# Kernel optimization log

Measured on AMD Instinct MI355X. Metric: run time of the kernel, lower is better.

## Reference

```python
import jax, jax.numpy as jnp
import numpy as np

B = 8192
H = 1024            # hidden_size
A = 512             # alphabet_size
S = 2               # sequence_length
D_IN = A * S        # 1024, gate input dim
D1, D2 = H // 2, H // 3   # decoder dims: 512, 341
TEMP = 1.0


def _linear_params(key, out_d, in_d):
    kw, kb = jax.random.split(key)
    lim = 1.0 / np.sqrt(in_d)
    W = jax.random.uniform(kw, (out_d, in_d), minval=-lim, maxval=lim, dtype=jnp.float32)
    b = jax.random.uniform(kb, (out_d,), minval=-lim, maxval=lim, dtype=jnp.float32)
    return W, b


def setup_inputs() -> dict:
    key = jax.random.key(0)
    ks = jax.random.split(key, 16)
    inp = {
        'x': jax.random.normal(ks[0], (B, D_IN), dtype=jnp.float32),
        'h': jax.random.normal(ks[1], (B, H), dtype=jnp.float32),
        'c': jax.random.normal(ks[2], (B, H), dtype=jnp.float32),
    }
    names = [('W_fi', 'b_fi', H, D_IN), ('W_fh', 'b_fh', H, H),
             ('W_ii', 'b_ii', H, D_IN), ('W_ih', 'b_ih', H, H),
             ('W_si', 'b_si', H, D_IN), ('W_sh', 'b_sh', H, H),
             ('W_oi', 'b_oi', H, D_IN), ('W_oh', 'b_oh', H, H),
             ('W_d1', 'b_d1', D1, H), ('W_d2', 'b_d2', D2, D1),
             ('W_d3', 'b_d3', A, D2)]
    for k, (wn, bn, od, idm) in zip(ks[3:3 + len(names)], names):
        W, b = _linear_params(k, od, idm)
        inp[wn] = W
        inp[bn] = b
    return inp


def reference(x, h, c,
              W_fi, b_fi, W_fh, b_fh,
              W_ii, b_ii, W_ih, b_ih,
              W_si, b_si, W_sh, b_sh,
              W_oi, b_oi, W_oh, b_oh,
              W_d1, b_d1, W_d2, b_d2, W_d3, b_d3):
    def lin(v, W, b):
        return v @ W.T + b

    f = jax.nn.sigmoid(lin(x, W_fi, b_fi) + lin(h, W_fh, b_fh))
    i = jax.nn.sigmoid(lin(x, W_ii, b_ii) + lin(h, W_ih, b_ih))
    s = jnp.tanh(lin(x, W_si, b_si) + lin(h, W_sh, b_sh))
    o = jax.nn.sigmoid(lin(x, W_oi, b_oi) + lin(h, W_oh, b_oh))
    c_new = c * f + i * s
    h_new = o * jnp.tanh(c_new)
    d = jnp.tanh(lin(h_new, W_d1, b_d1))
    d = jnp.tanh(lin(d, W_d2, b_d2))
    d = jax.nn.softmax(lin(d, W_d3, b_d3) / TEMP, axis=-1)
    return h_new, d
```

## Files before the change

### kernel.cpp

```cpp
#include <hip/hip_runtime.h>
#include <cstdint>
#include <cstddef>


typedef _Float16 half_t;
typedef _Float16 half8 __attribute__((ext_vector_type(8)));
typedef _Float16 half4v __attribute__((ext_vector_type(4)));
typedef float float4v __attribute__((ext_vector_type(4)));

#define GLD_LDS16(gptr, lptr)                                                  \
  __builtin_amdgcn_global_load_lds(                                            \
      (const __attribute__((address_space(1))) void*)(gptr),                   \
      (__attribute__((address_space(3))) void*)(lptr), 16, 0, 0)

__device__ __forceinline__ float fsig(float x) {
  return 1.0f / (1.0f + __expf(-x));
}
__device__ __forceinline__ float ftanh_(float x) {
  const float e = __expf(2.0f * x);
  return 1.0f - 2.0f / (e + 1.0f);
}

__global__ __launch_bounds__(256) void gemm_gates(const half_t* __restrict__ A,
                                                  const half_t* __restrict__ Bw,
                                                  const float* __restrict__ bias,
                                                  const float* __restrict__ cin,
                                                  float* __restrict__ hout,
                                                  half_t* __restrict__ h2f) {
  constexpr int K = 2048;
  __shared__ alignas(16) half_t As[128 * 32];
  __shared__ alignas(16) half_t Bs[128 * 32];
  const int tid = threadIdx.x;
  const int lane = tid & 63;
  const int wave = tid >> 6;
  const int m = lane & 15;
  const int q = lane >> 4;
  const int sx = (m >> 1) & 3;

  const int bid = blockIdx.x;
  const int xcd = bid & 7;
  const int l = bid >> 3;
  const size_t tile_n = (size_t)((xcd << 2) | (l & 3)) * 128;
  const size_t tile_m = (size_t)(l >> 2) * 128;
  const int wm = (wave >> 1) * 64;
  const int wn = (wave & 1) * 64;

  const int cA0 = tid, rA0 = cA0 >> 2, kA0 = ((cA0 & 3) ^ ((rA0 >> 1) & 3));
  const int cA1 = 256 + tid, rA1 = cA1 >> 2, kA1 = ((cA1 & 3) ^ ((rA1 >> 1) & 3));
  const half_t* Ag0 = A + (tile_m + rA0) * (size_t)K + kA0 * 8;
  const half_t* Ag1 = A + (tile_m + rA1) * (size_t)K + kA1 * 8;
  const half_t* Bg0 = Bw + (tile_n + rA0) * (size_t)K + kA0 * 8;
  const half_t* Bg1 = Bw + (tile_n + rA1) * (size_t)K + kA1 * 8;
  const int p0 = cA0 * 16, p1 = cA1 * 16;

  float4v acc[4][4] = {};
  for (int k0 = 0; k0 < K; k0 += 32) {
    __syncthreads();
    GLD_LDS16(Ag0 + k0, (char*)As + p0);
    GLD_LDS16(Ag1 + k0, (char*)As + p1);
    GLD_LDS16(Bg0 + k0, (char*)Bs + p0);
    GLD_LDS16(Bg1 + k0, (char*)Bs + p1);
    __syncthreads();
    const int ks = (q ^ sx) * 8;
    half8 af[4], bf[4];
#pragma unroll
    for (int i = 0; i < 4; ++i)
      af[i] = *(const half8*)(As + (wm + i * 16 + m) * 32 + ks);
#pragma unroll
    for (int j = 0; j < 4; ++j)
      bf[j] = *(const half8*)(Bs + (wn + j * 16 + m) * 32 + ks);
#pragma unroll
    for (int i = 0; i < 4; ++i)
#pragma unroll
      for (int j = 0; j < 4; ++j)
        acc[i][j] =
            __builtin_amdgcn_mfma_f32_16x16x32_f16(af[i], bf[j], acc[i][j], 0, 0, 0);
  }

  const int nwave = (int)tile_n + wn;
  const int u = ((nwave >> 6) << 4) + m;
  const int rtb = (int)((tile_m + wm) >> 4);
  const int ubase = (u >> 5) * 512 + ((u >> 3) & 3) * 128 + (u & 7);
  float bg[4];
#pragma unroll
  for (int g = 0; g < 4; ++g) bg[g] = bias[nwave + g * 16 + m];
#pragma unroll
  for (int i = 0; i < 4; ++i) {
#pragma unroll
    for (int r = 0; r < 4; ++r) {
      const size_t row = tile_m + wm + q * 4 + i * 16 + r;
      const size_t off = row * 1024 + u;
      const float F = fsig(acc[i][0][r] + bg[0]);
      const float I = fsig(acc[i][1][r] + bg[1]);
      const float S = ftanh_(acc[i][2][r] + bg[2]);
      const float O = fsig(acc[i][3][r] + bg[3]);
      const float cn = cin[off] * F + I * S;
      const float hn = O * ftanh_(cn);
      hout[off] = hn;
      h2f[(size_t)(rtb + i) * 16384 + ubase + (q * 4 + r) * 8] = (half_t)hn;
    }
  }
}

template <int K, int OUTK, int MODE>
__global__ __launch_bounds__(256) void dec_layer(const half_t* __restrict__ Af,
                                                 const half_t* __restrict__ W,
                                                 const float* __restrict__ bias,
                                                 void* __restrict__ outp) {
  constexpr int KP = K + 8;
  constexpr int CH = K / 8;
  constexpr int ITER = 32 * CH / 256;
  __shared__ alignas(16) half_t Wl[32 * KP];
  const int tid = threadIdx.x;
  const int lane = tid & 63;
  const int w = tid >> 6;
  const int m = lane & 15;
  const int q = lane >> 4;
  const int g = blockIdx.x;

#pragma unroll
  for (int it = 0; it < ITER; ++it) {
    const int ci = it * 256 + tid;
    const int c = ci / CH;
    const int kq = ci - c * CH;
    const half8 v = *(const half8*)(W + ((size_t)(g * 32 + c)) * K + kq * 8);
    *(half8*)(Wl + c * KP + kq * 8) = v;
  }
  __syncthreads();

  const int rt0 = blockIdx.y * 8 + w * 2;
  const half_t* a0 = Af + (size_t)rt0 * (16 * K) + lane * 8;
  const half_t* a1 = a0 + 16 * K;
  float4v acc[2][2] = {};
#pragma unroll 2
  for (int kk = 0; kk < K; kk += 32) {
    const half8 af0 = *(const half8*)(a0 + kk * 16);
    const half8 af1 = *(const half8*)(a1 + kk * 16);
    half8 bf[2];
#pragma unroll
    for (int j = 0; j < 2; ++j)
      bf[j] = *(const half8*)(Wl + (j * 16 + m) * KP + kk + q * 8);
    acc[0][0] = __builtin_amdgcn_mfma_f32_16x16x32_f16(af0, bf[0], acc[0][0], 0, 0, 0);
    acc[0][1] = __builtin_amdgcn_mfma_f32_16x16x32_f16(af0, bf[1], acc[0][1], 0, 0, 0);
    acc[1][0] = __builtin_amdgcn_mfma_f32_16x16x32_f16(af1, bf[0], acc[1][0], 0, 0, 0);
    acc[1][1] = __builtin_amdgcn_mfma_f32_16x16x32_f16(af1, bf[1], acc[1][1], 0, 0, 0);
  }

#pragma unroll
  for (int t = 0; t < 2; ++t) {
    const int rt = rt0 + t;
#pragma unroll
    for (int j = 0; j < 2; ++j) {
      const int col = g * 32 + j * 16 + m;
      const float bv = bias[col];
      if (MODE == 0) {
        half_t* of = (half_t*)outp;
        const size_t base = (size_t)rt * (16 * OUTK) + g * 512 +
                            (j * 2 + (m >> 3)) * 128 + (m & 7);
#pragma unroll
        for (int r = 0; r < 4; ++r)
          of[base + (q * 4 + r) * 8] = (half_t)ftanh_(acc[t][j][r] + bv);
      } else {
        float* ol = (float*)outp;
#pragma unroll
        for (int r = 0; r < 4; ++r)
          ol[((size_t)rt * 16 + q * 4 + r) * 512 + col] = acc[t][j][r] + bv;
      }
    }
  }
}

__global__ __launch_bounds__(256) void softmax512(const float* __restrict__ logits,
                                                  float* __restrict__ out) {
  const int row = blockIdx.x * 4 + (threadIdx.x >> 6);
  const int lane = threadIdx.x & 63;
  const float4v* src = (const float4v*)(logits + (size_t)row * 512);
  const float4v v0 = src[lane * 2];
  const float4v v1 = src[lane * 2 + 1];
  float mx = fmaxf(fmaxf(fmaxf(v0.x, v0.y), fmaxf(v0.z, v0.w)),
                   fmaxf(fmaxf(v1.x, v1.y), fmaxf(v1.z, v1.w)));
#pragma unroll
  for (int off = 32; off > 0; off >>= 1) mx = fmaxf(mx, __shfl_xor(mx, off, 64));
  const float e0 = __expf(v0.x - mx), e1 = __expf(v0.y - mx);
  const float e2 = __expf(v0.z - mx), e3 = __expf(v0.w - mx);
  const float e4 = __expf(v1.x - mx), e5 = __expf(v1.y - mx);
  const float e6 = __expf(v1.z - mx), e7 = __expf(v1.w - mx);
  float sum = ((e0 + e1) + (e2 + e3)) + ((e4 + e5) + (e6 + e7));
#pragma unroll
  for (int off = 32; off > 0; off >>= 1) sum += __shfl_xor(sum, off, 64);
  const float inv = 1.0f / sum;
  float4v o0, o1;
  o0.x = e0 * inv; o0.y = e1 * inv; o0.z = e2 * inv; o0.w = e3 * inv;
  o1.x = e4 * inv; o1.y = e5 * inv; o1.z = e6 * inv; o1.w = e7 * inv;
  float4v* dst = (float4v*)(out + (size_t)row * 512);
  dst[lane * 2] = o0;
  dst[lane * 2 + 1] = o1;
}

__global__ void prep_pack(const float* __restrict__ x, const float* __restrict__ h,
                          const float* __restrict__ Wfi, const float* __restrict__ Wfh,
                          const float* __restrict__ Wii, const float* __restrict__ Wih,
                          const float* __restrict__ Wsi, const float* __restrict__ Wsh,
                          const float* __restrict__ Woi, const float* __restrict__ Woh,
                          half_t* __restrict__ xh, half_t* __restrict__ wall) {
  const int bid = blockIdx.x;
  const float* src;
  half_t* dst;
  size_t idx;
  if (bid < 16384) {
    idx = ((size_t)bid * 256 + threadIdx.x) * 4;
    const size_t b = idx >> 11;
    const int col = (int)(idx & 2047);
    src = (col < 1024) ? (x + b * 1024 + col) : (h + b * 1024 + (col - 1024));
    dst = xh + idx;
  } else {
    idx = ((size_t)(bid - 16384) * 256 + threadIdx.x) * 4;
    const int n = (int)(idx >> 11);
    const int col = (int)(idx & 2047);
    const int g = (n >> 4) & 3;
    const size_t u = (size_t)(((n >> 6) << 4) | (n & 15));
    const float* Wi = (g == 0) ? Wfi : (g == 1) ? Wii : (g == 2) ? Wsi : Woi;
    const float* Wh = (g == 0) ? Wfh : (g == 1) ? Wih : (g == 2) ? Wsh : Woh;
    src = (col < 1024) ? (Wi + u * 1024 + col) : (Wh + u * 1024 + (col - 1024));
    dst = wall + idx;
  }
  const float4v v = *(const float4v*)src;
  half4v o;
  o.x = (half_t)v.x; o.y = (half_t)v.y; o.z = (half_t)v.z; o.w = (half_t)v.w;
  *(half4v*)dst = o;
}

__global__ void prep_small(const float* __restrict__ Wd1, const float* __restrict__ Wd2,
                           const float* __restrict__ Wd3, const float* __restrict__ bd2,
                           const float* __restrict__ bfi, const float* __restrict__ bfh,
                           const float* __restrict__ bii, const float* __restrict__ bih,
                           const float* __restrict__ bsi, const float* __restrict__ bsh,
                           const float* __restrict__ boi, const float* __restrict__ boh,
                           half_t* __restrict__ WD1, half_t* __restrict__ WD2h,
                           half_t* __restrict__ WD3h, float* __restrict__ BALL,
                           float* __restrict__ BD2) {
  const int bid = blockIdx.x;
  const int tid = threadIdx.x;
  if (bid < 512) {
    const size_t i4 = ((size_t)bid * 256 + tid) * 4;
    const float4v v = *(const float4v*)(Wd1 + i4);
    half4v o;
    o.x = (half_t)v.x; o.y = (half_t)v.y; o.z = (half_t)v.z; o.w = (half_t)v.w;
    *(half4v*)(WD1 + i4) = o;
  } else if (bid < 704) {
    const size_t i4 = ((size_t)(bid - 512) * 256 + tid) * 4;
    const int r = (int)(i4 >> 9);
    const int cc = (int)(i4 & 511);
    half4v o;
    if (r < 341) {
      const float4v v = *(const float4v*)(Wd2 + (size_t)r * 512 + cc);
      o.x = (half_t)v.x; o.y = (half_t)v.y; o.z = (half_t)v.z; o.w = (half_t)v.w;
    } else {
      o.x = (half_t)0.f; o.y = (half_t)0.f; o.z = (half_t)0.f; o.w = (half_t)0.f;
    }
    *(half4v*)(WD2h + i4) = o;
  } else if (bid < 896) {
    const size_t i4 = ((size_t)(bid - 704) * 256 + tid) * 4;
    const int r = (int)(i4 / 384);
    const int cc = (int)(i4 - (size_t)r * 384);
    half4v o;
    o.x = (cc + 0 < 341) ? (half_t)Wd3[(size_t)r * 341 + cc + 0] : (half_t)0.f;
    o.y = (cc + 1 < 341) ? (half_t)Wd3[(size_t)r * 341 + cc + 1] : (half_t)0.f;
    o.z = (cc + 2 < 341) ? (half_t)Wd3[(size_t)r * 341 + cc + 2] : (half_t)0.f;
    o.w = (cc + 3 < 341) ? (half_t)Wd3[(size_t)r * 341 + cc + 3] : (half_t)0.f;
    *(half4v*)(WD3h + i4) = o;
  } else if (bid < 912) {
    const int n = (bid - 896) * 256 + tid;
    const int g = (n >> 4) & 3;
    const int u = ((n >> 6) << 4) | (n & 15);
    const float* bi = (g == 0) ? bfi : (g == 1) ? bii : (g == 2) ? bsi : boi;
    const float* bh = (g == 0) ? bfh : (g == 1) ? bih : (g == 2) ? bsh : boh;
    BALL[n] = bi[u] + bh[u];
  } else {
    const int i = (bid - 912) * 256 + tid;
    if (i < 384) BD2[i] = (i < 341) ? bd2[i] : 0.0f;
  }
}

extern "C" void kernel_launch(void* const* d_in, const int* in_sizes, int n_in,
                              void* d_out, int out_size, void* d_ws, size_t ws_size,
                              hipStream_t stream) {
  const float* x = (const float*)d_in[0];
  const float* h = (const float*)d_in[1];
  const float* c = (const float*)d_in[2];
  const float* Wfi = (const float*)d_in[3];  const float* bfi = (const float*)d_in[4];
  const float* Wfh = (const float*)d_in[5];  const float* bfh = (const float*)d_in[6];
  const float* Wii = (const float*)d_in[7];  const float* bii = (const float*)d_in[8];
  const float* Wih = (const float*)d_in[9];  const float* bih = (const float*)d_in[10];
  const float* Wsi = (const float*)d_in[11]; const float* bsi = (const float*)d_in[12];
  const float* Wsh = (const float*)d_in[13]; const float* bsh = (const float*)d_in[14];
  const float* Woi = (const float*)d_in[15]; const float* boi = (const float*)d_in[16];
  const float* Woh = (const float*)d_in[17]; const float* boh = (const float*)d_in[18];
  const float* Wd1 = (const float*)d_in[19]; const float* bd1 = (const float*)d_in[20];
  const float* Wd2 = (const float*)d_in[21]; const float* bd2 = (const float*)d_in[22];
  const float* Wd3 = (const float*)d_in[23]; const float* bd3 = (const float*)d_in[24];

  char* ws = (char*)d_ws;
  size_t o = 0;
  auto alloc = [&](size_t bytes) {
    size_t cur = o;
    o += (bytes + 255) & ~(size_t)255;
    return cur;
  };
  half_t* XH   = (half_t*)(ws + alloc((size_t)8192 * 2048 * 2));
  half_t* WALL = (half_t*)(ws + alloc((size_t)4096 * 2048 * 2));
  float*  BALL = (float*)(ws + alloc(4096 * 4));
  half_t* WD1  = (half_t*)(ws + alloc((size_t)512 * 1024 * 2));
  half_t* WD2  = (half_t*)(ws + alloc((size_t)384 * 512 * 2));
  float*  BD2  = (float*)(ws + alloc(384 * 4));
  half_t* WD3  = (half_t*)(ws + alloc((size_t)512 * 384 * 2));
  half_t* H2F  = (half_t*)(ws + alloc((size_t)8192 * 1024 * 2));
  half_t* D1F  = (half_t*)(ws + alloc((size_t)8192 * 512 * 2));
  half_t* D2F  = (half_t*)(ws + alloc((size_t)8192 * 384 * 2));
  float*  LOG  = (float*)XH;

  float* h_out = (float*)d_out;
  float* d_outp = (float*)d_out + (size_t)8192 * 1024;

  prep_pack<<<24576, 256, 0, stream>>>(x, h, Wfi, Wfh, Wii, Wih, Wsi, Wsh, Woi, Woh,
                                       XH, WALL);
  prep_small<<<914, 256, 0, stream>>>(Wd1, Wd2, Wd3, bd2, bfi, bfh, bii, bih, bsi, bsh,
                                      boi, boh, WD1, WD2, WD3, BALL, BD2);

  gemm_gates<<<2048, 256, 0, stream>>>(XH, WALL, BALL, c, h_out, H2F);

  dec_layer<1024, 512, 0><<<dim3(16, 64), 256, 0, stream>>>(H2F, WD1, bd1, D1F);
  dec_layer<512, 384, 0><<<dim3(12, 64), 256, 0, stream>>>(D1F, WD2, BD2, D2F);
  dec_layer<384, 512, 1><<<dim3(16, 64), 256, 0, stream>>>(D2F, WD3, bd3, LOG);
  softmax512<<<2048, 256, 0, stream>>>(LOG, d_outp);
}
```

Baseline: 440.0 us.

## Enlarge gate GEMM tiles to 256x256 with triple-buffered async LDS pipeline

The fused gate GEMM moves from 128x128 tiles with 256 threads to 256x256 tiles with 512 threads, and each wave now computes a 128x64 sub-tile. Global-to-LDS loads become triple-buffered, prefetching two k-steps ahead and interleaving them with MFMA phases using explicit waitcnt, barriers and setprio. This targets the single-buffered load/compute serialization and the low reuse of the smaller tile. In exchange it uses much more LDS and more accumulator registers per thread, which can lower occupancy.

```diff
diff --git a/kernel.cpp b/kernel.cpp
--- a/kernel.cpp
+++ b/kernel.cpp
@@ -21,60 +21,110 @@
   return 1.0f - 2.0f / (e + 1.0f);
 }
 
-__global__ __launch_bounds__(256) void gemm_gates(const half_t* __restrict__ A,
-                                                  const half_t* __restrict__ Bw,
-                                                  const float* __restrict__ bias,
-                                                  const float* __restrict__ cin,
-                                                  float* __restrict__ hout,
-                                                  half_t* __restrict__ h2f) {
+__global__ __launch_bounds__(512, 2) void gemm_gates(const half_t* __restrict__ A,
+                                                     const half_t* __restrict__ Bw,
+                                                     const float* __restrict__ bias,
+                                                     const float* __restrict__ cin,
+                                                     float* __restrict__ hout,
+                                                     half_t* __restrict__ h2f) {
   constexpr int K = 2048;
-  __shared__ alignas(16) half_t As[128 * 32];
-  __shared__ alignas(16) half_t Bs[128 * 32];
+  constexpr int NT = 64;
+  __shared__ alignas(16) half_t As[3][256 * 32];
+  __shared__ alignas(16) half_t Bs[3][256 * 32];
   const int tid = threadIdx.x;
   const int lane = tid & 63;
   const int wave = tid >> 6;
   const int m = lane & 15;
   const int q = lane >> 4;
-  const int sx = (m >> 1) & 3;
+  const int ks = (q ^ ((m >> 1) & 3)) << 3;
+  const int wm = (wave >> 2) << 7;
+  const int wn = (wave & 3) << 6;
 
   const int bid = blockIdx.x;
   const int xcd = bid & 7;
   const int l = bid >> 3;
-  const size_t tile_n = (size_t)((xcd << 2) | (l & 3)) * 128;
-  const size_t tile_m = (size_t)(l >> 2) * 128;
-  const int wm = (wave >> 1) * 64;
-  const int wn = (wave & 1) * 64;
-
-  const int cA0 = tid, rA0 = cA0 >> 2, kA0 = ((cA0 & 3) ^ ((rA0 >> 1) & 3));
-  const int cA1 = 256 + tid, rA1 = cA1 >> 2, kA1 = ((cA1 & 3) ^ ((rA1 >> 1) & 3));
-  const half_t* Ag0 = A + (tile_m + rA0) * (size_t)K + kA0 * 8;
-  const half_t* Ag1 = A + (tile_m + rA1) * (size_t)K + kA1 * 8;
-  const half_t* Bg0 = Bw + (tile_n + rA0) * (size_t)K + kA0 * 8;
-  const half_t* Bg1 = Bw + (tile_n + rA1) * (size_t)K + kA1 * 8;
-  const int p0 = cA0 * 16, p1 = cA1 * 16;
-
-  float4v acc[4][4] = {};
-  for (int k0 = 0; k0 < K; k0 += 32) {
-    __syncthreads();
-    GLD_LDS16(Ag0 + k0, (char*)As + p0);
-    GLD_LDS16(Ag1 + k0, (char*)As + p1);
-    GLD_LDS16(Bg0 + k0, (char*)Bs + p0);
-    GLD_LDS16(Bg1 + k0, (char*)Bs + p1);
-    __syncthreads();
-    const int ks = (q ^ sx) * 8;
+  const size_t tile_n = (size_t)((xcd << 1) | (l & 1)) << 8;
+  const size_t tile_m = (size_t)(l >> 1) << 8;
+
+  const int ci0 = tid, ci1 = tid + 512;
+  const int r0 = ci0 >> 2, k0s = (ci0 & 3) ^ ((r0 >> 1) & 3);
+  const int r1 = ci1 >> 2, k1s = (ci1 & 3) ^ ((r1 >> 1) & 3);
+  const half_t* Ag0 = A + (tile_m + r0) * (size_t)K + k0s * 8;
+  const half_t* Ag1 = A + (tile_m + r1) * (size_t)K + k1s * 8;
+  const half_t* Bg0 = Bw + (tile_n + r0) * (size_t)K + k0s * 8;
+  const half_t* Bg1 = Bw + (tile_n + r1) * (size_t)K + k1s * 8;
+  const int p0 = ci0 * 16, p1 = ci1 * 16;
+
+  GLD_LDS16(Ag0, (char*)As[0] + p0);
+  GLD_LDS16(Ag1, (char*)As[0] + p1);
+  GLD_LDS16(Bg0, (char*)Bs[0] + p0);
+  GLD_LDS16(Bg1, (char*)Bs[0] + p1);
+  GLD_LDS16(Ag0 + 32, (char*)As[1] + p0);
+  GLD_LDS16(Ag1 + 32, (char*)As[1] + p1);
+  GLD_LDS16(Bg0 + 32, (char*)Bs[1] + p0);
+  GLD_LDS16(Bg1 + 32, (char*)Bs[1] + p1);
+  asm volatile("s_waitcnt vmcnt(4)" ::: "memory");
+  __builtin_amdgcn_s_barrier();
+  __builtin_amdgcn_sched_barrier(0);
+
+  float4v acc[8][4] = {};
+  int bc = 0;
+  for (int t = 0; t < NT; ++t) {
+    const half_t* as = As[bc];
+    const half_t* bs = Bs[bc];
+    const int bst = (bc + 2 >= 3) ? bc - 1 : bc + 2;
+    const size_t koff = (size_t)(t + 2) * 32;
     half8 af[4], bf[4];
 #pragma unroll
     for (int i = 0; i < 4; ++i)
-      af[i] = *(const half8*)(As + (wm + i * 16 + m) * 32 + ks);
+      af[i] = *(const half8*)(as + (wm + i * 16 + m) * 32 + ks);
 #pragma unroll
     for (int j = 0; j < 4; ++j)
-      bf[j] = *(const half8*)(Bs + (wn + j * 16 + m) * 32 + ks);
+      bf[j] = *(const half8*)(bs + (wn + j * 16 + m) * 32 + ks);
+    if (t < NT - 2) {
+      GLD_LDS16(Ag0 + koff, (char*)As[bst] + p0);
+      GLD_LDS16(Ag1 + koff, (char*)As[bst] + p1);
+    }
+    __builtin_amdgcn_s_barrier();
+    asm volatile("s_waitcnt lgkmcnt(0)" ::: "memory");
+    __builtin_amdgcn_sched_barrier(0);
+    __builtin_amdgcn_s_setprio(1);
 #pragma unroll
     for (int i = 0; i < 4; ++i)
 #pragma unroll
       for (int j = 0; j < 4; ++j)
-        acc[i][j] =
-            __builtin_amdgcn_mfma_f32_16x16x32_f16(af[i], bf[j], acc[i][j], 0, 0, 0);
+        acc[i][j] = __builtin_amdgcn_mfma_f32_16x16x32_f16(af[i], bf[j],
+                                                           acc[i][j], 0, 0, 0);
+    __builtin_amdgcn_s_setprio(0);
+    __builtin_amdgcn_s_barrier();
+    __builtin_amdgcn_sched_barrier(0);
+    half8 ag[4];
+#pragma unroll
+    for (int i = 0; i < 4; ++i)
+      ag[i] = *(const half8*)(as + (wm + 64 + i * 16 + m) * 32 + ks);
+    if (t < NT - 2) {
+      GLD_LDS16(Bg0 + koff, (char*)Bs[bst] + p0);
+      GLD_LDS16(Bg1 + koff, (char*)Bs[bst] + p1);
+    }
+    __builtin_amdgcn_s_barrier();
+    asm volatile("s_waitcnt lgkmcnt(0)" ::: "memory");
+    __builtin_amdgcn_sched_barrier(0);
+    __builtin_amdgcn_s_setprio(1);
+#pragma unroll
+    for (int i = 0; i < 4; ++i)
+#pragma unroll
+      for (int j = 0; j < 4; ++j)
+        acc[4 + i][j] = __builtin_amdgcn_mfma_f32_16x16x32_f16(
+            ag[i], bf[j], acc[4 + i][j], 0, 0, 0);
+    __builtin_amdgcn_s_setprio(0);
+    if (t < NT - 2) {
+      asm volatile("s_waitcnt vmcnt(4)" ::: "memory");
+    } else if (t == NT - 2) {
+      asm volatile("s_waitcnt vmcnt(0)" ::: "memory");
+    }
+    __builtin_amdgcn_s_barrier();
+    __builtin_amdgcn_sched_barrier(0);
+    bc = (bc + 1 == 3) ? 0 : bc + 1;
   }
 
   const int nwave = (int)tile_n + wn;
@@ -85,7 +135,7 @@
 #pragma unroll
   for (int g = 0; g < 4; ++g) bg[g] = bias[nwave + g * 16 + m];
 #pragma unroll
-  for (int i = 0; i < 4; ++i) {
+  for (int i = 0; i < 8; ++i) {
 #pragma unroll
     for (int r = 0; r < 4; ++r) {
       const size_t row = tile_m + wm + q * 4 + i * 16 + r;
@@ -327,7 +377,7 @@
   prep_small<<<914, 256, 0, stream>>>(Wd1, Wd2, Wd3, bd2, bfi, bfh, bii, bih, bsi, bsh,
                                       boi, boh, WD1, WD2, WD3, BALL, BD2);
 
-  gemm_gates<<<2048, 256, 0, stream>>>(XH, WALL, BALL, c, h_out, H2F);
+  gemm_gates<<<512, 512, 0, stream>>>(XH, WALL, BALL, c, h_out, H2F);
 
   dec_layer<1024, 512, 0><<<dim3(16, 64), 256, 0, stream>>>(H2F, WD1, bd1, D1F);
   dec_layer<512, 384, 0><<<dim3(12, 64), 256, 0, stream>>>(D1F, WD2, BD2, D2F);
```

New measurement: 403.9 us. -8.2%, faster.
